# Optimization experiments

Hardware: AMD Instinct MI355X
Metric: run time of the kernel (lower is better)

The kernel has to match this reference:

```python
import jax, jax.numpy as jnp
import numpy as np

B, FDIM, H, E = 16384, 512, 256, 128  # batch, feature_dim, lstm hidden, scenario encoding


def setup_inputs() -> dict:
    key = jax.random.key(0)
    ks = jax.random.split(key, 24)
    p = lambda k, shape: (jax.random.normal(k, shape, jnp.float32) * 0.05)
    return {
        "base_timeline": jax.random.normal(ks[0], (B, FDIM), jnp.float32),
        "counterfactual_scenario": jax.random.normal(ks[1], (B, FDIM), jnp.float32),
        # scenario_encoder: Linear(512,256) -> ReLU -> Linear(256,128)
        "w_se1": p(ks[2], (256, FDIM)), "b_se1": p(ks[3], (256,)),
        "w_se2": p(ks[4], (E, 256)), "b_se2": p(ks[5], (E,)),
        # LSTM layer 0: input 128, hidden 256 (gate order i,f,g,o)
        "w_ih0": p(ks[6], (4 * H, E)), "w_hh0": p(ks[7], (4 * H, H)),
        "b_ih0": p(ks[8], (4 * H,)), "b_hh0": p(ks[9], (4 * H,)),
        # LSTM layer 1: input 256, hidden 256
        "w_ih1": p(ks[10], (4 * H, H)), "w_hh1": p(ks[11], (4 * H, H)),
        "b_ih1": p(ks[12], (4 * H,)), "b_hh1": p(ks[13], (4 * H,)),
        # outcome_modifier: Linear(384,256) -> ReLU -> Linear(256,512) -> Tanh
        "w_om1": p(ks[14], (256, H + E)), "b_om1": p(ks[15], (256,)),
        "w_om2": p(ks[16], (FDIM, 256)), "b_om2": p(ks[17], (FDIM,)),
        # probability_estimator: Linear(512,128) -> ReLU -> Linear(128,1) -> Sigmoid
        "w_pe1": p(ks[18], (E, FDIM)), "b_pe1": p(ks[19], (E,)),
        "w_pe2": p(ks[20], (1, E)), "b_pe2": p(ks[21], (1,)),
        "num_steps": 10,
    }


def _lstm_cell(x_pre, h, c, w_hh, b_hh):
    gates = x_pre + h @ w_hh.T + b_hh  # [B, 4H]
    i, f, g, o = jnp.split(gates, 4, axis=-1)
    c = jax.nn.sigmoid(f) * c + jax.nn.sigmoid(i) * jnp.tanh(g)
    h = jax.nn.sigmoid(o) * jnp.tanh(c)
    return h, c


def reference(base_timeline, counterfactual_scenario,
              w_se1, b_se1, w_se2, b_se2,
              w_ih0, w_hh0, b_ih0, b_hh0,
              w_ih1, w_hh1, b_ih1, b_hh1,
              w_om1, b_om1, w_om2, b_om2,
              w_pe1, b_pe1, w_pe2, b_pe2,
              num_steps):
    # scenario encoding [B, 128]
    s = jax.nn.relu(counterfactual_scenario @ w_se1.T + b_se1) @ w_se2.T + b_se2
    bsz = base_timeline.shape[0]
    h = w_hh0.shape[1]
    # LSTM layer-0 input is the same scenario encoding each step -> precompute
    x_pre0 = s @ w_ih0.T + b_ih0  # [B, 4H]

    def step(carry, _):
        cur, h0, c0, h1, c1 = carry
        h0, c0 = _lstm_cell(x_pre0, h0, c0, w_hh0, b_hh0)
        x1 = h0 @ w_ih1.T + b_ih1
        h1, c1 = _lstm_cell(x1, h1, c1, w_hh1, b_hh1)
        comb = jnp.concatenate([h1, s], axis=-1)  # [B, 384]
        mod = jnp.tanh(jax.nn.relu(comb @ w_om1.T + b_om1) @ w_om2.T + b_om2)
        nxt = cur + 0.1 * mod
        prob = jax.nn.sigmoid(jax.nn.relu(nxt @ w_pe1.T + b_pe1) @ w_pe2.T + b_pe2)
        return (nxt, h0, c0, h1, c1), (nxt, prob)

    z = jnp.zeros((bsz, h), base_timeline.dtype)
    (final, _, _, _, _), (states, probs) = jax.lax.scan(
        step, (base_timeline, z, z, z, z), None, length=num_steps)
    alternate_timeline = jnp.swapaxes(states, 0, 1)        # [B, num_steps, 512]
    timeline_probabilities = jnp.swapaxes(probs, 0, 1)     # [B, num_steps, 1]
    return alternate_timeline, timeline_probabilities, s, final
```

## Files before the change

kernel.cpp:

```cpp
#include <hip/hip_runtime.h>

typedef short bf16x8 __attribute__((ext_vector_type(8)));
typedef float f32x4 __attribute__((ext_vector_type(4)));

#define DEV __device__ __forceinline__

DEV short f2bf(float f) {
  union { float f; unsigned u; } v; v.f = f;
  unsigned r = v.u + 0x7FFFu + ((v.u >> 16) & 1u);
  return (short)(r >> 16);
}
DEV float bf2f(short s) {
  union { unsigned u; float f; } v; v.u = ((unsigned)(unsigned short)s) << 16;
  return v.f;
}
DEV float sigm(float x) { return 1.0f / (1.0f + __expf(-x)); }
DEV float tanh_(float x) {
  float a = fabsf(x);
  float e = __expf(-2.0f * a);
  float t = (1.0f - e) / (1.0f + e);
  return copysignf(t, x);
}

#define LDS_S   0
#define LDS_H0  16384
#define LDS_H1  49152
#define LDS_T   81920
#define LDS_CF  16384
#define LDS_SZ  114688

#define OFF_SE1 0
#define OFF_SE2 131072
#define OFF_W0  163840
#define OFF_W1  557056
#define OFF_OM1 1081344
#define OFF_OM2 1179648
#define OFF_PE1 1310720

__global__ void prep_frag(const float* __restrict__ srcA, const float* __restrict__ srcB,
                          short* __restrict__ dst, int N, int K, int ksplit)
{
  const int e = blockIdx.x * 256 + threadIdx.x;
  if (e >= N * K) return;
  const int f = e >> 9;
  const int rix = e & 511;
  const int lane = rix >> 3, j = rix & 7;
  const int KK = K >> 5;
  const int ntile = f / KK, kk = f - ntile * KK;
  const int n = ntile * 16 + (lane & 15);
  const int k = kk * 32 + ((lane >> 4) << 3) + j;
  float v;
  if (k < ksplit) v = srcA[(size_t)n * ksplit + k];
  else            v = srcB[(size_t)n * (K - ksplit) + (k - ksplit)];
  dst[e] = f2bf(v);
}

template<int NT, int MT>
DEV void zacc(f32x4 (&acc)[NT][MT]) {
  #pragma unroll
  for (int n = 0; n < NT; ++n)
    #pragma unroll
    for (int m = 0; m < MT; ++m)
      acc[n][m] = (f32x4){0.f, 0.f, 0.f, 0.f};
}

template<int KK, int NT, int MT>
DEV void mm_tiles(const char* sm, int aBase0, int aStride0, int splitKB,
                  int aBase1, int aStride1,
                  const short* __restrict__ wf, int ntBase, int ntStride,
                  f32x4 (&acc)[NT][MT], int lane)
{
  const int l15 = lane & 15, l4 = lane >> 4;
  #pragma unroll
  for (int kk = 0; kk < KK; ++kk) {
    const int kb = kk * 64 + l4 * 16;
    bf16x8 a[MT];
    #pragma unroll
    for (int m = 0; m < MT; ++m) {
      const int r = m * 16 + l15;
      int off;
      if (kb < splitKB) off = aBase0 + r * aStride0 + (kb ^ ((r & 7) << 4));
      else              off = aBase1 + r * aStride1 + ((kb - splitKB) ^ ((r & 7) << 4));
      a[m] = *(const bf16x8*)(sm + off);
    }
    #pragma unroll
    for (int nt = 0; nt < NT; ++nt) {
      const bf16x8 b = *(const bf16x8*)(wf + (size_t)((ntBase + nt * ntStride) * KK + kk) * 512 + lane * 8);
      #pragma unroll
      for (int m = 0; m < MT; ++m)
        acc[nt][m] = __builtin_amdgcn_mfma_f32_16x16x32_bf16(a[m], b, acc[nt][m], 0, 0, 0);
    }
  }
}

DEV void lstm_ew(f32x4 (&acc)[4][4], f32x4 bv, float (&cp)[16], unsigned (&hp)[16], int hoff)
{
  #pragma unroll
  for (int m = 0; m < 4; ++m)
    #pragma unroll
    for (int q = 0; q < 4; ++q) {
      const float gi = acc[0][m][q] + bv[0];
      const float gf = acc[1][m][q] + bv[1];
      const float gg = acc[2][m][q] + bv[2];
      const float go = acc[3][m][q] + bv[3];
      const float c = sigm(gf) * cp[m * 4 + q] + sigm(gi) * tanh_(gg);
      cp[m * 4 + q] = c;
      const float h = sigm(go) * tanh_(c);
      const unsigned hb = (unsigned)(unsigned short)f2bf(h);
      const int pi = hoff + m * 2 + (q >> 1);
      if ((q & 1) == 0) hp[pi] = hb; else hp[pi] |= (hb << 16);
    }
}

__global__ __launch_bounds__(512, 2) void atg_main(
    const float* __restrict__ base, const float* __restrict__ cf,
    const float* __restrict__ b_se1, const float* __restrict__ b_se2,
    const float* __restrict__ b_ih0, const float* __restrict__ b_hh0,
    const float* __restrict__ b_ih1, const float* __restrict__ b_hh1,
    const float* __restrict__ b_om1, const float* __restrict__ b_om2,
    const short* __restrict__ wsb,
    float* __restrict__ outStates, float* __restrict__ outS,
    float* __restrict__ outFinal, int nsteps)
{
  __shared__ __align__(16) char sm[LDS_SZ];
  const int tid = threadIdx.x;
  const int lane = tid & 63, wid = tid >> 6;
  const int l15 = lane & 15, l4 = lane >> 4;
  const int row0 = blockIdx.x * 64;

  {
    const int r = tid >> 3, ci = tid & 7;
    const float* src = cf + (size_t)(row0 + r) * 512;
    #pragma unroll
    for (int i = 0; i < 16; ++i) {
      const int c = ci * 4 + i * 32;
      const float4 v = *(const float4*)(src + c);
      short4 h; h.x = f2bf(v.x); h.y = f2bf(v.y); h.z = f2bf(v.z); h.w = f2bf(v.w);
      *(short4*)(sm + LDS_CF + r * 1024 + ((c * 2) ^ ((r & 7) << 4))) = h;
    }
  }
  __syncthreads();

  {
    f32x4 acc[2][4]; zacc(acc);
    mm_tiles<16, 2, 4>(sm, LDS_CF, 1024, 1024, LDS_CF, 1024, wsb + OFF_SE1, wid * 2, 1, acc, lane);
    #pragma unroll
    for (int nt = 0; nt < 2; ++nt) {
      const int cc = wid * 32 + nt * 16 + l15;
      const float bv = b_se1[cc];
      #pragma unroll
      for (int m = 0; m < 4; ++m)
        #pragma unroll
        for (int q = 0; q < 4; ++q) {
          const int rr = m * 16 + l4 * 4 + q;
          const float u = fmaxf(acc[nt][m][q] + bv, 0.0f);
          *(short*)(sm + LDS_T + rr * 512 + ((cc * 2) ^ ((rr & 7) << 4))) = f2bf(u);
        }
    }
  }
  __syncthreads();

  {
    f32x4 acc[1][4]; zacc(acc);
    mm_tiles<8, 1, 4>(sm, LDS_T, 512, 512, LDS_T, 512, wsb + OFF_SE2, wid, 1, acc, lane);
    const int cc = wid * 16 + l15;
    const float bv = b_se2[cc];
    #pragma unroll
    for (int m = 0; m < 4; ++m)
      #pragma unroll
      for (int q = 0; q < 4; ++q) {
        const int rr = m * 16 + l4 * 4 + q;
        const float v = acc[0][m][q] + bv;
        outS[(size_t)(row0 + rr) * 128 + cc] = v;
        *(short*)(sm + LDS_S + rr * 256 + ((cc * 2) ^ ((rr & 7) << 4))) = f2bf(v);
      }
    #pragma unroll
    for (int i = 0; i < 8; ++i)
      *(f32x4*)(sm + LDS_H0 + tid * 128 + i * 16) = (f32x4){0.f, 0.f, 0.f, 0.f};
  }
  __syncthreads();

  f32x4 b0v[2], b1v[2], bo1v, bo2v;
  #pragma unroll
  for (int js = 0; js < 2; ++js) {
    f32x4 t0, t1;
    #pragma unroll
    for (int g = 0; g < 4; ++g) {
      const int c = g * 256 + wid * 32 + js * 16 + l15;
      t0[g] = b_ih0[c] + b_hh0[c];
      t1[g] = b_ih1[c] + b_hh1[c];
    }
    b0v[js] = t0; b1v[js] = t1;
  }
  {
    f32x4 t = (f32x4){0.f, 0.f, 0.f, 0.f};
    #pragma unroll
    for (int nt = 0; nt < 2; ++nt) t[nt] = b_om1[wid * 32 + nt * 16 + l15];
    bo1v = t;
    #pragma unroll
    for (int nt = 0; nt < 4; ++nt) t[nt] = b_om2[wid * 64 + nt * 16 + l15];
    bo2v = t;
  }

  float c0a[16], c0b[16], c1a[16], c1b[16];
  #pragma unroll
  for (int i = 0; i < 16; ++i) { c0a[i] = 0.f; c0b[i] = 0.f; c1a[i] = 0.f; c1b[i] = 0.f; }

  for (int step = 0; step < nsteps; ++step) {
    unsigned hp[16];
    {
      f32x4 acc[4][4]; zacc(acc);
      mm_tiles<12, 4, 4>(sm, LDS_S, 256, 256, LDS_H0, 512, wsb + OFF_W0, wid * 2 + 0, 16, acc, lane);
      lstm_ew(acc, b0v[0], c0a, hp, 0);
    }
    {
      f32x4 acc[4][4]; zacc(acc);
      mm_tiles<12, 4, 4>(sm, LDS_S, 256, 256, LDS_H0, 512, wsb + OFF_W0, wid * 2 + 1, 16, acc, lane);
      lstm_ew(acc, b0v[1], c0b, hp, 8);
    }
    __syncthreads();
    #pragma unroll
    for (int js = 0; js < 2; ++js)
      #pragma unroll
      for (int m = 0; m < 4; ++m)
        #pragma unroll
        for (int q = 0; q < 4; ++q) {
          const int rr = m * 16 + l4 * 4 + q;
          const int cc = wid * 32 + js * 16 + l15;
          const unsigned v = hp[js * 8 + m * 2 + (q >> 1)] >> ((q & 1) * 16);
          *(short*)(sm + LDS_H0 + rr * 512 + ((cc * 2) ^ ((rr & 7) << 4))) = (short)v;
        }
    __syncthreads();
    {
      f32x4 acc[4][4]; zacc(acc);
      mm_tiles<16, 4, 4>(sm, LDS_H0, 512, 512, LDS_H1, 512, wsb + OFF_W1, wid * 2 + 0, 16, acc, lane);
      lstm_ew(acc, b1v[0], c1a, hp, 0);
    }
    {
      f32x4 acc[4][4]; zacc(acc);
      mm_tiles<16, 4, 4>(sm, LDS_H0, 512, 512, LDS_H1, 512, wsb + OFF_W1, wid * 2 + 1, 16, acc, lane);
      lstm_ew(acc, b1v[1], c1b, hp, 8);
    }
    __syncthreads();
    #pragma unroll
    for (int js = 0; js < 2; ++js)
      #pragma unroll
      for (int m = 0; m < 4; ++m)
        #pragma unroll
        for (int q = 0; q < 4; ++q) {
          const int rr = m * 16 + l4 * 4 + q;
          const int cc = wid * 32 + js * 16 + l15;
          const unsigned v = hp[js * 8 + m * 2 + (q >> 1)] >> ((q & 1) * 16);
          *(short*)(sm + LDS_H1 + rr * 512 + ((cc * 2) ^ ((rr & 7) << 4))) = (short)v;
        }
    __syncthreads();
    {
      f32x4 acc[2][4]; zacc(acc);
      mm_tiles<12, 2, 4>(sm, LDS_H1, 512, 512, LDS_S, 256, wsb + OFF_OM1, wid * 2, 1, acc, lane);
      #pragma unroll
      for (int nt = 0; nt < 2; ++nt)
        #pragma unroll
        for (int m = 0; m < 4; ++m)
          #pragma unroll
          for (int q = 0; q < 4; ++q) {
            const int rr = m * 16 + l4 * 4 + q;
            const int cc = wid * 32 + nt * 16 + l15;
            const float u = fmaxf(acc[nt][m][q] + bo1v[nt], 0.0f);
            *(short*)(sm + LDS_T + rr * 512 + ((cc * 2) ^ ((rr & 7) << 4))) = f2bf(u);
          }
    }
    __syncthreads();
    {
      f32x4 acc[4][4]; zacc(acc);
      mm_tiles<8, 4, 4>(sm, LDS_T, 512, 512, LDS_T, 512, wsb + OFF_OM2, wid * 4, 1, acc, lane);
      #pragma unroll
      for (int nt = 0; nt < 4; ++nt)
        #pragma unroll
        for (int m = 0; m < 4; ++m)
          #pragma unroll
          for (int q = 0; q < 4; ++q) {
            const int rr = m * 16 + l4 * 4 + q;
            const int rg = row0 + rr;
            const int cc = wid * 64 + nt * 16 + l15;
            const float curv = (step == 0) ? base[(size_t)rg * 512 + cc]
                                           : outStates[((size_t)rg * nsteps + (step - 1)) * 512 + cc];
            const float nx = curv + 0.1f * tanh_(acc[nt][m][q] + bo2v[nt]);
            outStates[((size_t)rg * nsteps + step) * 512 + cc] = nx;
            if (step == nsteps - 1) outFinal[(size_t)rg * 512 + cc] = nx;
          }
    }
  }
}

#define PE_AS 0
#define PE_P1 32768
#define PE_W2 40960
#define PE_LDS 41472

__global__ __launch_bounds__(512, 4) void atg_pe(
    const float* __restrict__ states, float* __restrict__ probs,
    const float* __restrict__ b_pe1, const float* __restrict__ w_pe2,
    const float* __restrict__ b_pe2, const short* __restrict__ wpe1f, int totrows)
{
  __shared__ __align__(16) char sm[PE_LDS];
  const int tid = threadIdx.x;
  const int lane = tid & 63, wid = tid >> 6;
  const int l15 = lane & 15, l4 = lane >> 4;
  const int row0 = blockIdx.x * 32;

  {
    const int r = tid >> 4, ci = tid & 15;
    const float* src = states + (size_t)(row0 + r) * 512;
    #pragma unroll
    for (int i = 0; i < 8; ++i) {
      const int c = ci * 4 + i * 64;
      const float4 v = *(const float4*)(src + c);
      short4 h; h.x = f2bf(v.x); h.y = f2bf(v.y); h.z = f2bf(v.z); h.w = f2bf(v.w);
      *(short4*)(sm + PE_AS + r * 1024 + ((c * 2) ^ ((r & 7) << 4))) = h;
    }
  }
  if (tid < 128) *(float*)(sm + PE_W2 + tid * 4) = w_pe2[tid];
  __syncthreads();

  {
    f32x4 acc[1][2]; zacc(acc);
    mm_tiles<16, 1, 2>(sm, PE_AS, 1024, 1024, PE_AS, 1024, wpe1f, wid, 1, acc, lane);
    const int cc = wid * 16 + l15;
    const float bv = b_pe1[cc];
    #pragma unroll
    for (int m = 0; m < 2; ++m)
      #pragma unroll
      for (int q = 0; q < 4; ++q) {
        const int rr = m * 16 + l4 * 4 + q;
        const float u = fmaxf(acc[0][m][q] + bv, 0.0f);
        *(short*)(sm + PE_P1 + rr * 256 + ((cc * 2) ^ ((rr & 7) << 4))) = f2bf(u);
      }
  }
  __syncthreads();

  {
    const int r = tid >> 4, ci = tid & 15;
    const int kb = ci * 16;
    const bf16x8 pv = *(const bf16x8*)(sm + PE_P1 + r * 256 + (kb ^ ((r & 7) << 4)));
    float s = 0.0f;
    #pragma unroll
    for (int j = 0; j < 8; ++j)
      s += bf2f(pv[j]) * *(const float*)(sm + PE_W2 + (ci * 8 + j) * 4);
    #pragma unroll
    for (int d = 8; d >= 1; d >>= 1)
      s += __shfl_down(s, d, 16);
    if (ci == 0 && (row0 + r) < totrows)
      probs[row0 + r] = 1.0f / (1.0f + __expf(-(s + b_pe2[0])));
  }
}

extern "C" void kernel_launch(void* const* d_in, const int* in_sizes, int n_in,
                              void* d_out, int out_size, void* d_ws, size_t ws_size,
                              hipStream_t stream)
{
  const float* base  = (const float*)d_in[0];
  const float* cf    = (const float*)d_in[1];
  const float* w_se1 = (const float*)d_in[2];
  const float* b_se1 = (const float*)d_in[3];
  const float* w_se2 = (const float*)d_in[4];
  const float* b_se2 = (const float*)d_in[5];
  const float* w_ih0 = (const float*)d_in[6];
  const float* w_hh0 = (const float*)d_in[7];
  const float* b_ih0 = (const float*)d_in[8];
  const float* b_hh0 = (const float*)d_in[9];
  const float* w_ih1 = (const float*)d_in[10];
  const float* w_hh1 = (const float*)d_in[11];
  const float* b_ih1 = (const float*)d_in[12];
  const float* b_hh1 = (const float*)d_in[13];
  const float* w_om1 = (const float*)d_in[14];
  const float* b_om1 = (const float*)d_in[15];
  const float* w_om2 = (const float*)d_in[16];
  const float* b_om2 = (const float*)d_in[17];
  const float* w_pe1 = (const float*)d_in[18];
  const float* b_pe1 = (const float*)d_in[19];
  const float* w_pe2 = (const float*)d_in[20];
  const float* b_pe2 = (const float*)d_in[21];

  const int B = in_sizes[0] / 512;
  const long nsteps = ((long)out_size - (long)B * 640) / ((long)B * 513);
  short* wsb = (short*)d_ws;
  float* out = (float*)d_out;

  auto prep = [&](const float* A, const float* Bp, long off, int N, int K, int ks) {
    const int total = N * K;
    prep_frag<<<dim3((total + 255) / 256), dim3(256), 0, stream>>>(A, Bp, wsb + off, N, K, ks);
  };
  prep(w_se1, w_se1, OFF_SE1, 256, 512, 512);
  prep(w_se2, w_se2, OFF_SE2, 128, 256, 256);
  prep(w_ih0, w_hh0, OFF_W0, 1024, 384, 128);
  prep(w_ih1, w_hh1, OFF_W1, 1024, 512, 256);
  prep(w_om1, w_om1, OFF_OM1, 256, 384, 384);
  prep(w_om2, w_om2, OFF_OM2, 512, 256, 256);
  prep(w_pe1, w_pe1, OFF_PE1, 128, 512, 512);

  float* outS = out + (size_t)B * nsteps * 513;
  float* outF = outS + (size_t)B * 128;
  atg_main<<<dim3(B / 64), dim3(512), 0, stream>>>(base, cf, b_se1, b_se2, b_ih0, b_hh0,
      b_ih1, b_hh1, b_om1, b_om2, wsb, out, outS, outF, (int)nsteps);

  const long totrows = (long)B * nsteps;
  float* probs = out + (size_t)B * nsteps * 512;
  atg_pe<<<dim3((int)(totrows / 32)), dim3(512), 0, stream>>>(out, probs, b_pe1, w_pe2, b_pe2,
      wsb + OFF_PE1, (int)totrows);
}
```

Before: 3.159 ms.

## Double-buffer weight fragment loads and pad fragment tiles in matmul loop

The weight fragment buffer is repacked with a 64-short pad per n-tile, and the offsets are recomputed to match. mm_tiles now prefetches the next k-step's B fragments into registers while the current step's MFMAs run, so global/L2 load latency can overlap with compute. The A-path split is disabled (split offset set very large) for single-source matmuls, which removes a per-iteration branch. Holding two sets of B fragments raises register pressure, which could lower occupancy.

```diff
diff --git a/kernel.cpp b/kernel.cpp
--- a/kernel.cpp
+++ b/kernel.cpp
@@ -30,12 +30,12 @@
 #define LDS_SZ  114688
 
 #define OFF_SE1 0
-#define OFF_SE2 131072
-#define OFF_W0  163840
-#define OFF_W1  557056
-#define OFF_OM1 1081344
-#define OFF_OM2 1179648
-#define OFF_PE1 1310720
+#define OFF_SE2 132096
+#define OFF_W0  165376
+#define OFF_W1  562688
+#define OFF_OM1 1091072
+#define OFF_OM2 1190400
+#define OFF_PE1 1323520
 
 __global__ void prep_frag(const float* __restrict__ srcA, const float* __restrict__ srcB,
                           short* __restrict__ dst, int N, int K, int ksplit)
@@ -52,7 +52,7 @@
   float v;
   if (k < ksplit) v = srcA[(size_t)n * ksplit + k];
   else            v = srcB[(size_t)n * (K - ksplit) + (k - ksplit)];
-  dst[e] = f2bf(v);
+  dst[(size_t)ntile * (KK * 512 + 64) + kk * 512 + rix] = f2bf(v);
 }
 
 template<int NT, int MT>
@@ -71,8 +71,21 @@
                   f32x4 (&acc)[NT][MT], int lane)
 {
   const int l15 = lane & 15, l4 = lane >> 4;
+  const short* wp = wf + lane * 8;
+  constexpr int PITCH = KK * 512 + 64;
+  bf16x8 b[2][NT];
+  #pragma unroll
+  for (int nt = 0; nt < NT; ++nt)
+    b[0][nt] = *(const bf16x8*)(wp + (size_t)(ntBase + nt * ntStride) * PITCH);
   #pragma unroll
   for (int kk = 0; kk < KK; ++kk) {
+    const int cb = kk & 1, nb = cb ^ 1;
+    if (kk + 1 < KK) {
+      #pragma unroll
+      for (int nt = 0; nt < NT; ++nt)
+        b[nb][nt] = *(const bf16x8*)(wp + (size_t)(ntBase + nt * ntStride) * PITCH
+                                        + (size_t)(kk + 1) * 512);
+    }
     const int kb = kk * 64 + l4 * 16;
     bf16x8 a[MT];
     #pragma unroll
@@ -84,12 +97,10 @@
       a[m] = *(const bf16x8*)(sm + off);
     }
     #pragma unroll
-    for (int nt = 0; nt < NT; ++nt) {
-      const bf16x8 b = *(const bf16x8*)(wf + (size_t)((ntBase + nt * ntStride) * KK + kk) * 512 + lane * 8);
+    for (int nt = 0; nt < NT; ++nt)
       #pragma unroll
       for (int m = 0; m < MT; ++m)
-        acc[nt][m] = __builtin_amdgcn_mfma_f32_16x16x32_bf16(a[m], b, acc[nt][m], 0, 0, 0);
-    }
+        acc[nt][m] = __builtin_amdgcn_mfma_f32_16x16x32_bf16(a[m], b[cb][nt], acc[nt][m], 0, 0, 0);
   }
 }
 
@@ -143,7 +154,7 @@
 
   {
     f32x4 acc[2][4]; zacc(acc);
-    mm_tiles<16, 2, 4>(sm, LDS_CF, 1024, 1024, LDS_CF, 1024, wsb + OFF_SE1, wid * 2, 1, acc, lane);
+    mm_tiles<16, 2, 4>(sm, LDS_CF, 1024, 1 << 28, LDS_CF, 1024, wsb + OFF_SE1, wid * 2, 1, acc, lane);
     #pragma unroll
     for (int nt = 0; nt < 2; ++nt) {
       const int cc = wid * 32 + nt * 16 + l15;
@@ -162,7 +173,7 @@
 
   {
     f32x4 acc[1][4]; zacc(acc);
-    mm_tiles<8, 1, 4>(sm, LDS_T, 512, 512, LDS_T, 512, wsb + OFF_SE2, wid, 1, acc, lane);
+    mm_tiles<8, 1, 4>(sm, LDS_T, 512, 1 << 28, LDS_T, 512, wsb + OFF_SE2, wid, 1, acc, lane);
     const int cc = wid * 16 + l15;
     const float bv = b_se2[cc];
     #pragma unroll
@@ -272,7 +283,7 @@
     __syncthreads();
     {
       f32x4 acc[4][4]; zacc(acc);
-      mm_tiles<8, 4, 4>(sm, LDS_T, 512, 512, LDS_T, 512, wsb + OFF_OM2, wid * 4, 1, acc, lane);
+      mm_tiles<8, 4, 4>(sm, LDS_T, 512, 1 << 28, LDS_T, 512, wsb + OFF_OM2, wid * 4, 1, acc, lane);
       #pragma unroll
       for (int nt = 0; nt < 4; ++nt)
         #pragma unroll
@@ -280,13 +291,13 @@
           #pragma unroll
           for (int q = 0; q < 4; ++q) {
             const int rr = m * 16 + l4 * 4 + q;
-            const int rg = row0 + rr;
+            const size_t rg = row0 + rr;
             const int cc = wid * 64 + nt * 16 + l15;
-            const float curv = (step == 0) ? base[(size_t)rg * 512 + cc]
-                                           : outStates[((size_t)rg * nsteps + (step - 1)) * 512 + cc];
+            const float curv = (step == 0) ? base[rg * 512 + cc]
+                                           : outStates[(rg * nsteps + (step - 1)) * 512 + cc];
             const float nx = curv + 0.1f * tanh_(acc[nt][m][q] + bo2v[nt]);
-            outStates[((size_t)rg * nsteps + step) * 512 + cc] = nx;
-            if (step == nsteps - 1) outFinal[(size_t)rg * 512 + cc] = nx;
+            outStates[(rg * nsteps + step) * 512 + cc] = nx;
+            if (step == nsteps - 1) outFinal[rg * 512 + cc] = nx;
           }
     }
   }
@@ -324,7 +335,7 @@
 
   {
     f32x4 acc[1][2]; zacc(acc);
-    mm_tiles<16, 1, 2>(sm, PE_AS, 1024, 1024, PE_AS, 1024, wpe1f, wid, 1, acc, lane);
+    mm_tiles<16, 1, 2>(sm, PE_AS, 1024, 1 << 28, PE_AS, 1024, wpe1f, wid, 1, acc, lane);
     const int cc = wid * 16 + l15;
     const float bv = b_pe1[cc];
     #pragma unroll
```

Result: slower. 3.294 ms (+4.2%).
